# Kernel tuning notes

Measured on AMD Instinct MI355X. Metric: run time of the kernel, lower is better.

The kernel has to match this reference:

```python
import jax, jax.numpy as jnp
import numpy as np


def setup_inputs() -> dict:
    key = jax.random.key(0)
    ks = jax.random.split(key, 6)
    B, N, D, H, W = 8, 16, 128, 64, 64
    x = jax.random.normal(ks[0], (B, N, D, H, W), dtype=jnp.float32)
    mask = jax.random.randint(ks[1], (B, N, H, W), 0, 2, dtype=jnp.int32)
    s = 1.0 / np.sqrt(D)
    Wq = jax.random.normal(ks[2], (D, D), dtype=jnp.float32) * s
    bq = jax.random.normal(ks[3], (D,), dtype=jnp.float32) * s
    Wk = jax.random.normal(ks[4], (D, D), dtype=jnp.float32) * s
    bk = jax.random.normal(ks[5], (D,), dtype=jnp.float32) * s
    return {"x": x, "mask": mask, "Wq": Wq, "bq": bq, "Wk": Wk, "bk": bk}


def reference(x, mask, Wq, bq, Wk, bk):
    B, N, D, H, W = x.shape
    K = H * W
    # (B, N, K, D) token view of spatial grid
    xr = jnp.transpose(x, (0, 1, 3, 4, 2)).reshape(B, N, K, D)
    m = mask.reshape(B, N, K, 1).astype(x.dtype)
    valid_count = jnp.sum(m, axis=2, keepdims=True)          # (B, N, 1, 1)
    mean_x = jnp.sum(xr * m, axis=2, keepdims=True) / valid_count  # (B, N, 1, D)
    # Linear layers: y = x @ W^T + b (torch convention)
    query = mean_x @ Wq.T + bq                               # (B, N, 1, D)
    keys = xr @ Wk.T + bk                                    # (B, N, K, D)
    attn = jnp.einsum('bnqd,bnkd->bnqk', query, keys)        # (B, N, 1, K)
    neg_inf = jnp.array(-jnp.inf, dtype=attn.dtype)
    attn = jnp.where(m.reshape(B, N, 1, K) == 0, neg_inf, attn)
    attn = jax.nn.softmax(attn / jnp.sqrt(jnp.asarray(D, attn.dtype)), axis=-1)
    pooled = jnp.einsum('bnqk,bnkd->bnqd', attn, xr)         # (B, N, 1, D)
    return pooled[:, :, 0, :]                                 # (B, N, D)
```

## Files before the change

### kernel.cpp

```cpp
#include <hip/hip_runtime.h>
#include <math.h>

#define G 128
#define D 128
#define K 4096
#define SPLITS 8
#define CHUNK 512


__global__ __launch_bounds__(256) void k0_init(float* __restrict__ meanacc_cnt,
                                               float* __restrict__ out) {
  int i = blockIdx.x * 256 + threadIdx.x;
  if (i < G * D + G) meanacc_cnt[i] = 0.0f;
  if (i < G * D) out[i] = 0.0f;
}

__global__ __launch_bounds__(256) void k1_mean(const float* __restrict__ x,
                                               const int* __restrict__ mask,
                                               float* __restrict__ meanacc,
                                               float* __restrict__ cnt) {
  const int g = blockIdx.x >> 3;
  const int s = blockIdx.x & 7;
  const int k0 = s * CHUNK;
  const int tid = threadIdx.x, wid = tid >> 6, lane = tid & 63;

  const int4* m4 = (const int4*)(mask + (size_t)g * K + k0);
  int4 mi0 = m4[lane];
  int4 mi1 = m4[lane + 64];
  float4 m0 = make_float4((float)mi0.x, (float)mi0.y, (float)mi0.z, (float)mi0.w);
  float4 m1 = make_float4((float)mi1.x, (float)mi1.y, (float)mi1.z, (float)mi1.w);

  if (wid == 0) {
    float cp = m0.x + m0.y + m0.z + m0.w + m1.x + m1.y + m1.z + m1.w;
#pragma unroll
    for (int o = 32; o > 0; o >>= 1) cp += __shfl_down(cp, o, 64);
    if (lane == 0) atomicAdd(cnt + g, cp);
  }

  const float4* x4 = (const float4*)x;
  const size_t gbase4 = (((size_t)g * D) * K + k0) >> 2;
  for (int d = wid; d < D; d += 4) {
    size_t r4 = gbase4 + (size_t)d * (K / 4);
    float4 a = x4[r4 + lane];
    float4 b = x4[r4 + lane + 64];
    float sum = a.x * m0.x + a.y * m0.y + a.z * m0.z + a.w * m0.w
              + b.x * m1.x + b.y * m1.y + b.z * m1.z + b.w * m1.w;
#pragma unroll
    for (int o = 32; o > 0; o >>= 1) sum += __shfl_down(sum, o, 64);
    if (lane == 0) atomicAdd(meanacc + g * D + d, sum);
  }
}

__global__ __launch_bounds__(128) void k2_query(const float* __restrict__ meanacc,
                                                const float* __restrict__ cnt,
                                                const float* __restrict__ Wq,
                                                const float* __restrict__ bq,
                                                const float* __restrict__ Wk,
                                                const float* __restrict__ bk,
                                                float* __restrict__ qt,
                                                float* __restrict__ cvec) {
  __shared__ float mean_s[D];
  __shared__ float query_s[D];
  __shared__ float red[D];
  const int g = blockIdx.x, t = threadIdx.x;
  float c = cnt[g];
  mean_s[t] = meanacc[g * D + t] / c;
  __syncthreads();
  float q = bq[t];
  for (int d2 = 0; d2 < D; ++d2) q += mean_s[d2] * Wq[t * D + d2];
  query_s[t] = q;
  red[t] = q * bk[t];
  __syncthreads();
  for (int o = 64; o > 0; o >>= 1) {
    if (t < o) red[t] += red[t + o];
    __syncthreads();
  }
  if (t == 0) cvec[g] = red[0];
  float qq = 0.0f;
  for (int d = 0; d < D; ++d) qq += query_s[d] * Wk[d * D + t];
  qt[g * D + t] = qq;
}

__global__ __launch_bounds__(256) void k3_logits(const float* __restrict__ x,
                                                 const int* __restrict__ mask,
                                                 const float* __restrict__ qt,
                                                 const float* __restrict__ cvec,
                                                 float* __restrict__ wlog) {
  __shared__ float qs[D];
  const int g = blockIdx.x >> 3;
  const int s = blockIdx.x & 7;
  const int k0 = s * CHUNK, t = threadIdx.x;
  if (t < D) qs[t] = qt[g * D + t];
  __syncthreads();
  const float c = cvec[g];
  const float2* xg2 = (const float2*)(x + (size_t)g * D * K + k0);
  float a0 = 0.0f, a1 = 0.0f;
  for (int d = 0; d < D; ++d) {
    float2 v = xg2[d * (K / 2) + t];
    a0 += qs[d] * v.x;
    a1 += qs[d] * v.y;
  }
  const float scale = 0.08838834764831845f;
  const int kk = g * K + k0 + 2 * t;
  int mm0 = mask[kk];
  int mm1 = mask[kk + 1];
  wlog[kk]     = mm0 ? (a0 + c) * scale : -INFINITY;
  wlog[kk + 1] = mm1 ? (a1 + c) * scale : -INFINITY;
}

__global__ __launch_bounds__(256) void k4_softmax(float* __restrict__ wlog,
                                                  float* __restrict__ denomv) {
  __shared__ float red[256];
  const int g = blockIdx.x, t = threadIdx.x;
  float4* l4 = (float4*)(wlog + (size_t)g * K);
  float4 v[4];
  float mx = -INFINITY;
#pragma unroll
  for (int i = 0; i < 4; ++i) {
    v[i] = l4[t + i * 256];
    mx = fmaxf(mx, fmaxf(fmaxf(v[i].x, v[i].y), fmaxf(v[i].z, v[i].w)));
  }
  red[t] = mx;
  __syncthreads();
  for (int o = 128; o > 0; o >>= 1) {
    if (t < o) red[t] = fmaxf(red[t], red[t + o]);
    __syncthreads();
  }
  mx = red[0];
  __syncthreads();
  float sm = 0.0f;
#pragma unroll
  for (int i = 0; i < 4; ++i) {
    v[i].x = __expf(v[i].x - mx);
    v[i].y = __expf(v[i].y - mx);
    v[i].z = __expf(v[i].z - mx);
    v[i].w = __expf(v[i].w - mx);
    sm += v[i].x + v[i].y + v[i].z + v[i].w;
    l4[t + i * 256] = v[i];
  }
  red[t] = sm;
  __syncthreads();
  for (int o = 128; o > 0; o >>= 1) {
    if (t < o) red[t] += red[t + o];
    __syncthreads();
  }
  if (t == 0) denomv[g] = red[0];
}

__global__ __launch_bounds__(256) void k5_pool(const float* __restrict__ x,
                                               const float* __restrict__ wlog,
                                               const float* __restrict__ denomv,
                                               float* __restrict__ out) {
  const int g = blockIdx.x >> 3;
  const int s = blockIdx.x & 7;
  const int k0 = s * CHUNK;
  const int tid = threadIdx.x, wid = tid >> 6, lane = tid & 63;
  const float inv = 1.0f / denomv[g];

  const float4* w4 = (const float4*)(wlog + (size_t)g * K + k0);
  float4 w0 = w4[lane];
  float4 w1 = w4[lane + 64];

  const float4* x4 = (const float4*)x;
  const size_t gbase4 = (((size_t)g * D) * K + k0) >> 2;
  for (int d = wid; d < D; d += 4) {
    size_t r4 = gbase4 + (size_t)d * (K / 4);
    float4 a = x4[r4 + lane];
    float4 b = x4[r4 + lane + 64];
    float sum = a.x * w0.x + a.y * w0.y + a.z * w0.z + a.w * w0.w
              + b.x * w1.x + b.y * w1.y + b.z * w1.z + b.w * w1.w;
#pragma unroll
    for (int o = 32; o > 0; o >>= 1) sum += __shfl_down(sum, o, 64);
    if (lane == 0) atomicAdd(out + g * D + d, sum * inv);
  }
}

extern "C" void kernel_launch(void* const* d_in, const int* in_sizes, int n_in,
                              void* d_out, int out_size, void* d_ws, size_t ws_size,
                              hipStream_t stream) {
  const float* x  = (const float*)d_in[0];
  const int* mask = (const int*)d_in[1];
  const float* Wq = (const float*)d_in[2];
  const float* bq = (const float*)d_in[3];
  const float* Wk = (const float*)d_in[4];
  const float* bk = (const float*)d_in[5];
  float* out = (float*)d_out;

  float* ws      = (float*)d_ws;
  float* meanacc = ws;
  float* cnt     = ws + G * D;
  float* qt      = ws + G * D + G;
  float* cvec    = ws + 2 * G * D + G;
  float* wlog    = ws + 2 * G * D + 2 * G;
  float* denomv  = ws + 2 * G * D + 2 * G + G * K;

  k0_init<<<(G * D + G + 255) / 256, 256, 0, stream>>>(meanacc, out);
  k1_mean<<<G * SPLITS, 256, 0, stream>>>(x, mask, meanacc, cnt);
  k2_query<<<G, 128, 0, stream>>>(meanacc, cnt, Wq, bq, Wk, bk, qt, cvec);
  k3_logits<<<G * SPLITS, 256, 0, stream>>>(x, mask, qt, cvec, wlog);
  k4_softmax<<<G, 256, 0, stream>>>(wlog, denomv);
  k5_pool<<<G * SPLITS, 256, 0, stream>>>(x, wlog, denomv, out);
}
```

Before: 459.0 us.

## Fuse logits, softmax and pooling into one pass over x tiles in shared memory

Merges the logits, softmax and pooling kernels into one kernel. Each block stages a 128x64 tile of x in shared memory, computes logits, exponentiates without max subtraction and accumulates both the weighted sum and the denominator with atomics. This reads x twice in total instead of three times and drops the global logits buffer. The mean kernel is also restructured to give each block four full-length rows with no atomics, and the mask count moves into the query kernel. The risk is overflow in exp because no running max is kept, and more atomic traffic from the larger number of blocks.

```diff
diff --git a/kernel.cpp b/kernel.cpp
--- a/kernel.cpp
+++ b/kernel.cpp
@@ -4,71 +4,74 @@
 #define G 128
 #define D 128
 #define K 4096
-#define SPLITS 8
-#define CHUNK 512
+#define CK 64
 
 
-__global__ __launch_bounds__(256) void k0_init(float* __restrict__ meanacc_cnt,
-                                               float* __restrict__ out) {
+__global__ __launch_bounds__(256) void k0_init(float* __restrict__ p, int n) {
   int i = blockIdx.x * 256 + threadIdx.x;
-  if (i < G * D + G) meanacc_cnt[i] = 0.0f;
-  if (i < G * D) out[i] = 0.0f;
+  if (i < n) p[i] = 0.0f;
 }
 
 __global__ __launch_bounds__(256) void k1_mean(const float* __restrict__ x,
                                                const int* __restrict__ mask,
-                                               float* __restrict__ meanacc,
-                                               float* __restrict__ cnt) {
-  const int g = blockIdx.x >> 3;
-  const int s = blockIdx.x & 7;
-  const int k0 = s * CHUNK;
-  const int tid = threadIdx.x, wid = tid >> 6, lane = tid & 63;
-
-  const int4* m4 = (const int4*)(mask + (size_t)g * K + k0);
-  int4 mi0 = m4[lane];
-  int4 mi1 = m4[lane + 64];
-  float4 m0 = make_float4((float)mi0.x, (float)mi0.y, (float)mi0.z, (float)mi0.w);
-  float4 m1 = make_float4((float)mi1.x, (float)mi1.y, (float)mi1.z, (float)mi1.w);
-
-  if (wid == 0) {
-    float cp = m0.x + m0.y + m0.z + m0.w + m1.x + m1.y + m1.z + m1.w;
+                                               float* __restrict__ meanacc) {
+  __shared__ float mf[K];
+  const int g = blockIdx.x >> 5;
+  const int dbase = (blockIdx.x & 31) * 4;
+  const int tid = threadIdx.x;
+  const int4* m4 = (const int4*)(mask + (size_t)g * K);
+  for (int i = tid; i < K / 4; i += 256) {
+    int4 mi = m4[i];
+    *(float4*)&mf[4 * i] =
+        make_float4((float)mi.x, (float)mi.y, (float)mi.z, (float)mi.w);
+  }
+  __syncthreads();
+  const int wid = tid >> 6, lane = tid & 63;
+  const int d = dbase + wid;
+  const float4* x4 = (const float4*)(x + ((size_t)g * D + d) * K);
+  const float4* mf4 = (const float4*)mf;
+  float4 acc = make_float4(0.f, 0.f, 0.f, 0.f);
 #pragma unroll
-    for (int o = 32; o > 0; o >>= 1) cp += __shfl_down(cp, o, 64);
-    if (lane == 0) atomicAdd(cnt + g, cp);
+  for (int it = 0; it < K / 256; ++it) {
+    float4 a = x4[it * 64 + lane];
+    float4 m = mf4[it * 64 + lane];
+    acc.x += a.x * m.x;
+    acc.y += a.y * m.y;
+    acc.z += a.z * m.z;
+    acc.w += a.w * m.w;
   }
-
-  const float4* x4 = (const float4*)x;
-  const size_t gbase4 = (((size_t)g * D) * K + k0) >> 2;
-  for (int d = wid; d < D; d += 4) {
-    size_t r4 = gbase4 + (size_t)d * (K / 4);
-    float4 a = x4[r4 + lane];
-    float4 b = x4[r4 + lane + 64];
-    float sum = a.x * m0.x + a.y * m0.y + a.z * m0.z + a.w * m0.w
-              + b.x * m1.x + b.y * m1.y + b.z * m1.z + b.w * m1.w;
+  float s = acc.x + acc.y + acc.z + acc.w;
 #pragma unroll
-    for (int o = 32; o > 0; o >>= 1) sum += __shfl_down(sum, o, 64);
-    if (lane == 0) atomicAdd(meanacc + g * D + d, sum);
-  }
+  for (int o = 32; o > 0; o >>= 1) s += __shfl_down(s, o, 64);
+  if (lane == 0) meanacc[g * D + d] = s;
 }
 
-__global__ __launch_bounds__(128) void k2_query(const float* __restrict__ meanacc,
-                                                const float* __restrict__ cnt,
-                                                const float* __restrict__ Wq,
-                                                const float* __restrict__ bq,
-                                                const float* __restrict__ Wk,
-                                                const float* __restrict__ bk,
-                                                float* __restrict__ qt,
-                                                float* __restrict__ cvec) {
-  __shared__ float mean_s[D];
-  __shared__ float query_s[D];
-  __shared__ float red[D];
+__global__ __launch_bounds__(128) void k2_query(
+    const float* __restrict__ meanacc, const int* __restrict__ mask,
+    const float* __restrict__ Wq, const float* __restrict__ bq,
+    const float* __restrict__ Wk, const float* __restrict__ bk,
+    float* __restrict__ qt, float* __restrict__ cvec) {
+  __shared__ float mean_s[D], query_s[D], red[D];
   const int g = blockIdx.x, t = threadIdx.x;
-  float c = cnt[g];
-  mean_s[t] = meanacc[g * D + t] / c;
+  const int4* m4 = (const int4*)(mask + (size_t)g * K);
+  int csum = 0;
+  for (int i = t; i < K / 4; i += 128) {
+    int4 v = m4[i];
+    csum += v.x + v.y + v.z + v.w;
+  }
+  red[t] = (float)csum;
+  __syncthreads();
+  for (int o = 64; o > 0; o >>= 1) {
+    if (t < o) red[t] += red[t + o];
+    __syncthreads();
+  }
+  const float cnt = red[0];
+  mean_s[t] = meanacc[g * D + t] / cnt;
   __syncthreads();
   float q = bq[t];
-  for (int d2 = 0; d2 < D; ++d2) q += mean_s[d2] * Wq[t * D + d2];
+  for (int d = 0; d < D; ++d) q += mean_s[d] * Wq[t * D + d];
   query_s[t] = q;
+  __syncthreads();
   red[t] = q * bk[t];
   __syncthreads();
   for (int o = 64; o > 0; o >>= 1) {
@@ -76,109 +79,71 @@
     __syncthreads();
   }
   if (t == 0) cvec[g] = red[0];
-  float qq = 0.0f;
+  float qq = 0.f;
   for (int d = 0; d < D; ++d) qq += query_s[d] * Wk[d * D + t];
   qt[g * D + t] = qq;
 }
 
-__global__ __launch_bounds__(256) void k3_logits(const float* __restrict__ x,
-                                                 const int* __restrict__ mask,
-                                                 const float* __restrict__ qt,
-                                                 const float* __restrict__ cvec,
-                                                 float* __restrict__ wlog) {
+__global__ __launch_bounds__(256) void k3_fused(
+    const float* __restrict__ x, const int* __restrict__ mask,
+    const float* __restrict__ qt, const float* __restrict__ cvec,
+    float* __restrict__ oacc, float* __restrict__ denom) {
+  __shared__ float xs[D][CK + 4];
   __shared__ float qs[D];
-  const int g = blockIdx.x >> 3;
-  const int s = blockIdx.x & 7;
-  const int k0 = s * CHUNK, t = threadIdx.x;
-  if (t < D) qs[t] = qt[g * D + t];
+  __shared__ float part_l[4][CK];
+  __shared__ float wsm[CK];
+  __shared__ float red[256];
+  const int g = blockIdx.x >> 6;
+  const int k0 = (blockIdx.x & 63) * CK;
+  const int tid = threadIdx.x;
+  if (tid < D) qs[tid] = qt[g * D + tid];
+  const float4* xg = (const float4*)(x + (size_t)g * D * K + k0);
+  for (int i = tid; i < D * (CK / 4); i += 256) {
+    int d = i >> 4, j = i & 15;
+    *(float4*)&xs[d][4 * j] = xg[(size_t)d * (K / 4) + j];
+  }
   __syncthreads();
-  const float c = cvec[g];
-  const float2* xg2 = (const float2*)(x + (size_t)g * D * K + k0);
-  float a0 = 0.0f, a1 = 0.0f;
-  for (int d = 0; d < D; ++d) {
-    float2 v = xg2[d * (K / 2) + t];
-    a0 += qs[d] * v.x;
-    a1 += qs[d] * v.y;
+  {
+    const int k = tid & 63, p = tid >> 6;
+    float s = 0.f;
+#pragma unroll 8
+    for (int d = p * 32; d < p * 32 + 32; ++d) s += qs[d] * xs[d][k];
+    part_l[p][k] = s;
   }
-  const float scale = 0.08838834764831845f;
-  const int kk = g * K + k0 + 2 * t;
-  int mm0 = mask[kk];
-  int mm1 = mask[kk + 1];
-  wlog[kk]     = mm0 ? (a0 + c) * scale : -INFINITY;
-  wlog[kk + 1] = mm1 ? (a1 + c) * scale : -INFINITY;
+  __syncthreads();
+  if (tid < CK) {
+    const float scale = 0.08838834764831845f;
+    float l = (part_l[0][tid] + part_l[1][tid] + part_l[2][tid] +
+               part_l[3][tid] + cvec[g]) * scale;
+    float w = mask[(size_t)g * K + k0 + tid] ? __expf(l) : 0.f;
+    wsm[tid] = w;
+#pragma unroll
+    for (int o = 32; o > 0; o >>= 1) w += __shfl_down(w, o, 64);
+    if (tid == 0) atomicAdd(denom + g, w);
+  }
+  __syncthreads();
+  {
+    const int d = tid & 127, h = tid >> 7;
+    float a = 0.f;
+#pragma unroll 8
+    for (int i = h * 32; i < h * 32 + 32; ++i) a += wsm[i] * xs[d][i];
+    red[tid] = a;
+  }
+  __syncthreads();
+  if (tid < D) atomicAdd(oacc + g * D + tid, red[tid] + red[tid + 128]);
 }
 
-__global__ __launch_bounds__(256) void k4_softmax(float* __restrict__ wlog,
-                                                  float* __restrict__ denomv) {
-  __shared__ float red[256];
-  const int g = blockIdx.x, t = threadIdx.x;
-  float4* l4 = (float4*)(wlog + (size_t)g * K);
-  float4 v[4];
-  float mx = -INFINITY;
-#pragma unroll
-  for (int i = 0; i < 4; ++i) {
-    v[i] = l4[t + i * 256];
-    mx = fmaxf(mx, fmaxf(fmaxf(v[i].x, v[i].y), fmaxf(v[i].z, v[i].w)));
-  }
-  red[t] = mx;
-  __syncthreads();
-  for (int o = 128; o > 0; o >>= 1) {
-    if (t < o) red[t] = fmaxf(red[t], red[t + o]);
-    __syncthreads();
-  }
-  mx = red[0];
-  __syncthreads();
-  float sm = 0.0f;
-#pragma unroll
-  for (int i = 0; i < 4; ++i) {
-    v[i].x = __expf(v[i].x - mx);
-    v[i].y = __expf(v[i].y - mx);
-    v[i].z = __expf(v[i].z - mx);
-    v[i].w = __expf(v[i].w - mx);
-    sm += v[i].x + v[i].y + v[i].z + v[i].w;
-    l4[t + i * 256] = v[i];
-  }
-  red[t] = sm;
-  __syncthreads();
-  for (int o = 128; o > 0; o >>= 1) {
-    if (t < o) red[t] += red[t + o];
-    __syncthreads();
-  }
-  if (t == 0) denomv[g] = red[0];
-}
-
-__global__ __launch_bounds__(256) void k5_pool(const float* __restrict__ x,
-                                               const float* __restrict__ wlog,
-                                               const float* __restrict__ denomv,
+__global__ __launch_bounds__(256) void k4_norm(const float* __restrict__ oacc,
+                                               const float* __restrict__ denom,
                                                float* __restrict__ out) {
-  const int g = blockIdx.x >> 3;
-  const int s = blockIdx.x & 7;
-  const int k0 = s * CHUNK;
-  const int tid = threadIdx.x, wid = tid >> 6, lane = tid & 63;
-  const float inv = 1.0f / denomv[g];
-
-  const float4* w4 = (const float4*)(wlog + (size_t)g * K + k0);
-  float4 w0 = w4[lane];
-  float4 w1 = w4[lane + 64];
-
-  const float4* x4 = (const float4*)x;
-  const size_t gbase4 = (((size_t)g * D) * K + k0) >> 2;
-  for (int d = wid; d < D; d += 4) {
-    size_t r4 = gbase4 + (size_t)d * (K / 4);
-    float4 a = x4[r4 + lane];
-    float4 b = x4[r4 + lane + 64];
-    float sum = a.x * w0.x + a.y * w0.y + a.z * w0.z + a.w * w0.w
-              + b.x * w1.x + b.y * w1.y + b.z * w1.z + b.w * w1.w;
-#pragma unroll
-    for (int o = 32; o > 0; o >>= 1) sum += __shfl_down(sum, o, 64);
-    if (lane == 0) atomicAdd(out + g * D + d, sum * inv);
-  }
+  int i = blockIdx.x * 256 + threadIdx.x;
+  out[i] = oacc[i] / denom[i >> 7];
 }
 
 extern "C" void kernel_launch(void* const* d_in, const int* in_sizes, int n_in,
-                              void* d_out, int out_size, void* d_ws, size_t ws_size,
-                              hipStream_t stream) {
-  const float* x  = (const float*)d_in[0];
+                              void* d_out, int out_size, void* d_ws,
+                              size_t ws_size, hipStream_t stream) {
+  const float* x = (const float*)d_in[0];
   const int* mask = (const int*)d_in[1];
   const float* Wq = (const float*)d_in[2];
   const float* bq = (const float*)d_in[3];
@@ -186,18 +151,16 @@
   const float* bk = (const float*)d_in[5];
   float* out = (float*)d_out;
 
-  float* ws      = (float*)d_ws;
+  float* ws = (float*)d_ws;
   float* meanacc = ws;
-  float* cnt     = ws + G * D;
-  float* qt      = ws + G * D + G;
-  float* cvec    = ws + 2 * G * D + G;
-  float* wlog    = ws + 2 * G * D + 2 * G;
-  float* denomv  = ws + 2 * G * D + 2 * G + G * K;
+  float* qt = ws + G * D;
+  float* cvec = ws + 2 * G * D;
+  float* oacc = ws + 2 * G * D + G;
+  float* denom = ws + 3 * G * D + G;
 
-  k0_init<<<(G * D + G + 255) / 256, 256, 0, stream>>>(meanacc, out);
-  k1_mean<<<G * SPLITS, 256, 0, stream>>>(x, mask, meanacc, cnt);
-  k2_query<<<G, 128, 0, stream>>>(meanacc, cnt, Wq, bq, Wk, bk, qt, cvec);
-  k3_logits<<<G * SPLITS, 256, 0, stream>>>(x, mask, qt, cvec, wlog);
-  k4_softmax<<<G, 256, 0, stream>>>(wlog, denomv);
-  k5_pool<<<G * SPLITS, 256, 0, stream>>>(x, wlog, denomv, out);
+  k0_init<<<(G * D + G + 255) / 256, 256, 0, stream>>>(oacc, G * D + G);
+  k1_mean<<<G * 32, 256, 0, stream>>>(x, mask, meanacc);
+  k2_query<<<G, 128, 0, stream>>>(meanacc, mask, Wq, bq, Wk, bk, qt, cvec);
+  k3_fused<<<G * (K / CK), 256, 0, stream>>>(x, mask, qt, cvec, oacc, denom);
+  k4_norm<<<(G * D) / 256, 256, 0, stream>>>(oacc, denom, out);
 }
```

Result: no change. 457.4 us (-0.4%).
